# Kernel optimization log

Measured on AMD Instinct MI355X. Metric: run time of the kernel, lower is better.

Reference implementation:

```python
import jax, jax.numpy as jnp
import numpy as np

N_ATOM = 4_000_000
N_FRAG = 200_000
EIG_THRESHOLD = 0.01


def setup_inputs() -> dict:
    key = jax.random.key(0)
    k1, k2, k3, k4, k5 = jax.random.split(key, 5)
    f_atom = jax.random.normal(k1, (N_ATOM, 3), jnp.float32)
    atom_pos = jax.random.normal(k2, (N_ATOM, 3), jnp.float32) * 5.0
    T_frag = jax.random.normal(k3, (N_FRAG, 3), jnp.float32) * 5.0
    frag_id = jax.random.randint(k4, (N_ATOM,), 0, N_FRAG)
    frag_sizes = jax.random.randint(k5, (N_FRAG,), 1, 40)
    return {"f_atom": f_atom, "atom_pos": atom_pos, "T_frag": T_frag,
            "frag_id": frag_id, "frag_sizes": frag_sizes, "n_frag": N_FRAG}


def reference(f_atom, atom_pos, T_frag, frag_id, frag_sizes, n_frag):
    dtype = f_atom.dtype
    # scatter_mean(f_atom, frag_id): segment_sum / counts
    counts = jax.ops.segment_sum(jnp.ones((f_atom.shape[0],), dtype), frag_id,
                                 num_segments=n_frag)
    denom = jnp.maximum(counts, 1.0)[:, None]
    v_frag = jax.ops.segment_sum(f_atom, frag_id, num_segments=n_frag) / denom  # [F,3]

    r_arm = atom_pos - T_frag[frag_id]                                   # [N,3]
    torque = jax.ops.segment_sum(jnp.cross(r_arm, f_atom), frag_id,
                                 num_segments=n_frag)                    # [F,3]

    r2 = jnp.sum(r_arm * r_arm, axis=-1)                                 # [N]
    I_diag = jax.ops.segment_sum(r2, frag_id, num_segments=n_frag)       # [F]
    rr = r_arm[:, :, None] * r_arm[:, None, :]                           # [N,3,3]
    I_off = jax.ops.segment_sum(rr.reshape(-1, 9), frag_id,
                                num_segments=n_frag).reshape(-1, 3, 3)   # [F,3,3]
    I_tensor = I_diag[:, None, None] * jnp.eye(3, dtype=dtype) - I_off   # [F,3,3]

    eigenvalues, eigenvectors = jnp.linalg.eigh(I_tensor)                # [F,3], [F,3,3]
    max_eig = jnp.maximum(jnp.max(eigenvalues, axis=-1, keepdims=True), 1e-8)
    observable = (eigenvalues > EIG_THRESHOLD * max_eig).astype(dtype)   # [F,3]
    observable = jnp.where((frag_sizes <= 1)[:, None],
                           jnp.zeros((), dtype), observable)

    torque_eig = jnp.einsum('nji,nj->ni', eigenvectors, torque)          # V^T torque
    omega_eig = torque_eig / jnp.maximum(eigenvalues, 1e-6) * observable
    omega_frag = jnp.einsum('nij,nj->ni', eigenvectors, omega_eig)
    P_observable = jnp.einsum('nij,nj,nkj->nik', eigenvectors, observable, eigenvectors)
    return v_frag, omega_frag, P_observable
```

## Files before the change

### kernel.cpp

```cpp
#include <hip/hip_runtime.h>
#include <math.h>

__device__ __forceinline__ void frag_epilogue(
    const float* a, int f, int n_frag, const int* __restrict__ frag_sizes,
    float* __restrict__ out)
{
    float cntf  = a[12];
    float denom = fmaxf(cntf, 1.0f);
    float vfx = a[0] / denom, vfy = a[1] / denom, vfz = a[2] / denom;

    double tq0 = (double)a[3], tq1 = (double)a[4], tq2 = (double)a[5];
    double Mxx = (double)a[6], Myy = (double)a[7], Mzz = (double)a[8];
    double Mxy = (double)a[9], Mxz = (double)a[10], Myz = (double)a[11];
    double tr = Mxx + Myy + Mzz;

    double A[3][3] = {
        { tr - Mxx, -Mxy,     -Mxz     },
        { -Mxy,     tr - Myy, -Myz     },
        { -Mxz,     -Myz,     tr - Mzz }
    };
    double V[3][3] = {{1,0,0},{0,1,0},{0,0,1}};

    for (int sweep = 0; sweep < 6; ++sweep) {
        for (int pq = 0; pq < 3; ++pq) {
            int p = (pq == 2) ? 1 : 0;
            int q = (pq == 0) ? 1 : 2;
            double apq = A[p][q];
            if (fabs(apq) <= 1e-14 * (fabs(A[p][p]) + fabs(A[q][q])) ||
                fabs(apq) < 1e-300) continue;
            double theta = (A[q][q] - A[p][p]) / (2.0 * apq);
            double tt;
            if (fabs(theta) > 1e100) tt = 1.0 / (2.0 * theta);
            else tt = copysign(1.0, theta) / (fabs(theta) + sqrt(theta * theta + 1.0));
            double c = 1.0 / sqrt(tt * tt + 1.0);
            double s = tt * c;
            double app = A[p][p], aqq = A[q][q];
            A[p][p] = app - tt * apq;
            A[q][q] = aqq + tt * apq;
            A[p][q] = 0.0; A[q][p] = 0.0;
            int r = 3 - p - q;
            double arp = A[r][p], arq = A[r][q];
            A[r][p] = c * arp - s * arq; A[p][r] = A[r][p];
            A[r][q] = s * arp + c * arq; A[q][r] = A[r][q];
            for (int i2 = 0; i2 < 3; ++i2) {
                double vip = V[i2][p], viq = V[i2][q];
                V[i2][p] = c * vip - s * viq;
                V[i2][q] = s * vip + c * viq;
            }
        }
    }

    double lam0 = A[0][0], lam1 = A[1][1], lam2 = A[2][2];
    double maxeig = fmax(fmax(fmax(lam0, lam1), lam2), 1e-8);
    double thr = 0.01 * maxeig;
    bool small_frag = (frag_sizes[f] <= 1);
    double o0 = (!small_frag && lam0 > thr) ? 1.0 : 0.0;
    double o1 = (!small_frag && lam1 > thr) ? 1.0 : 0.0;
    double o2 = (!small_frag && lam2 > thr) ? 1.0 : 0.0;

    double te0 = V[0][0]*tq0 + V[1][0]*tq1 + V[2][0]*tq2;
    double te1 = V[0][1]*tq0 + V[1][1]*tq1 + V[2][1]*tq2;
    double te2 = V[0][2]*tq0 + V[1][2]*tq1 + V[2][2]*tq2;
    double we0 = te0 / fmax(lam0, 1e-6) * o0;
    double we1 = te1 / fmax(lam1, 1e-6) * o1;
    double we2 = te2 / fmax(lam2, 1e-6) * o2;
    double w0 = V[0][0]*we0 + V[0][1]*we1 + V[0][2]*we2;
    double w1 = V[1][0]*we0 + V[1][1]*we1 + V[1][2]*we2;
    double w2 = V[2][0]*we0 + V[2][1]*we1 + V[2][2]*we2;

    size_t F = (size_t)n_frag;
    out[(size_t)f*3 + 0] = vfx;
    out[(size_t)f*3 + 1] = vfy;
    out[(size_t)f*3 + 2] = vfz;
    out[F*3 + (size_t)f*3 + 0] = (float)w0;
    out[F*3 + (size_t)f*3 + 1] = (float)w1;
    out[F*3 + (size_t)f*3 + 2] = (float)w2;

    float* P = out + F*6 + (size_t)f*9;
    #pragma unroll
    for (int i2 = 0; i2 < 3; ++i2)
        #pragma unroll
        for (int k = 0; k < 3; ++k)
            P[i2*3 + k] = (float)(V[i2][0]*o0*V[k][0] + V[i2][1]*o1*V[k][1]
                                  + V[i2][2]*o2*V[k][2]);
}

#define NBK  512
#define FPB  400
#define CAP2 2048
#define TILE 16
#define APB  (256 * TILE)
#define MAXPT 8
#define NCHUNK 16

__global__ __launch_bounds__(256) void count_atoms(
    const int* __restrict__ frag_id,
    unsigned*  __restrict__ histrows,
    int n_atom)
{
    __shared__ unsigned hist[NBK];
    int t = threadIdx.x;
    for (int b = t; b < NBK; b += 256) hist[b] = 0;
    __syncthreads();
    const int4* fid4 = (const int4*)frag_id;
    int bs4 = blockIdx.x * (APB / 4);
    #pragma unroll
    for (int j = 0; j < TILE / 4; ++j) {
        int i4 = bs4 + j * 256 + t;
        if (4 * i4 < n_atom) {
            int4 v = fid4[i4];
            atomicAdd(&hist[v.x / FPB], 1u);
            atomicAdd(&hist[v.y / FPB], 1u);
            atomicAdd(&hist[v.z / FPB], 1u);
            atomicAdd(&hist[v.w / FPB], 1u);
        }
    }
    __syncthreads();
    unsigned* row = histrows + (size_t)blockIdx.x * NBK;
    for (int b = t; b < NBK; b += 256) row[b] = hist[b];
}

__global__ __launch_bounds__(256) void scan_pass1(
    const unsigned* __restrict__ histrows,
    unsigned* __restrict__ chunksums,
    int nblk, int ch)
{
    int col = blockIdx.x * 256 + threadIdx.x;
    int c   = blockIdx.y;
    int r0 = c * ch, r1 = r0 + ch;
    if (r1 > nblk) r1 = nblk;
    unsigned s = 0;
    for (int r = r0; r < r1; ++r) s += histrows[(size_t)r * NBK + col];
    chunksums[(size_t)c * NBK + col] = s;
}

__global__ __launch_bounds__(256) void scan_pass2(
    unsigned* __restrict__ chunksums,
    unsigned* __restrict__ totals)
{
    int col = blockIdx.x * 256 + threadIdx.x;
    unsigned cum = 0;
    #pragma unroll
    for (int c = 0; c < NCHUNK; ++c) {
        size_t idx = (size_t)c * NBK + col;
        unsigned v = chunksums[idx];
        chunksums[idx] = cum;
        cum += v;
    }
    totals[col] = cum;
}

__global__ __launch_bounds__(256) void scan_pass3(
    unsigned* __restrict__ histrows,
    const unsigned* __restrict__ chunksums,
    int nblk, int ch)
{
    int col = blockIdx.x * 256 + threadIdx.x;
    int c   = blockIdx.y;
    int r0 = c * ch, r1 = r0 + ch;
    if (r1 > nblk) r1 = nblk;
    unsigned cum = chunksums[(size_t)c * NBK + col];
    for (int r = r0; r < r1; ++r) {
        size_t idx = (size_t)r * NBK + col;
        unsigned v = histrows[idx];
        histrows[idx] = cum;
        cum += v;
    }
}

__global__ __launch_bounds__(256) void scan_base(
    const unsigned* __restrict__ totals,
    unsigned* __restrict__ bucket_base)
{
    __shared__ unsigned part[256];
    int t = threadIdx.x;
    unsigned v0 = totals[2*t], v1 = totals[2*t + 1];
    part[t] = v0 + v1;
    __syncthreads();
    for (int st = 1; st < 256; st <<= 1) {
        unsigned v = (t >= st) ? part[t - st] : 0u;
        __syncthreads();
        part[t] += v;
        __syncthreads();
    }
    unsigned base = (t == 0) ? 0u : part[t - 1];
    bucket_base[2*t]     = base;
    bucket_base[2*t + 1] = base + v0;
    if (t == 255) bucket_base[NBK] = part[255];
}

__global__ __launch_bounds__(256) void scatter_atoms(
    const float* __restrict__ f_atom,
    const float* __restrict__ atom_pos,
    const int*   __restrict__ frag_id,
    const unsigned* __restrict__ histrows,
    const unsigned* __restrict__ bucket_base,
    float4*      __restrict__ recs,
    int n_atom)
{
    __shared__ unsigned hist[NBK];
    __shared__ unsigned obase[NBK];
    int t = threadIdx.x;
    for (int b = t; b < NBK; b += 256) hist[b] = 0;
    __syncthreads();

    const int4*   fid4 = (const int4*)frag_id;
    const float4* pos4 = (const float4*)atom_pos;
    const float4* ff4  = (const float4*)f_atom;
    int bs4 = blockIdx.x * (APB / 4);

    int4     fv[TILE / 4];
    unsigned rank[TILE];
    #pragma unroll
    for (int j = 0; j < TILE / 4; ++j) {
        int i4 = bs4 + j * 256 + t;
        if (4 * i4 < n_atom) {
            int4 v = fid4[i4];
            fv[j] = v;
            rank[4*j+0] = atomicAdd(&hist[v.x / FPB], 1u);
            rank[4*j+1] = atomicAdd(&hist[v.y / FPB], 1u);
            rank[4*j+2] = atomicAdd(&hist[v.z / FPB], 1u);
            rank[4*j+3] = atomicAdd(&hist[v.w / FPB], 1u);
        } else {
            fv[j].x = -1;
        }
    }
    const unsigned* row = histrows + (size_t)blockIdx.x * NBK;
    for (int b = t; b < NBK; b += 256) obase[b] = row[b] + bucket_base[b];
    __syncthreads();

    #pragma unroll
    for (int j = 0; j < TILE / 4; ++j) {
        if (fv[j].x < 0) continue;
        size_t i4 = (size_t)(bs4 + j * 256 + t);
        float4 p0 = pos4[3*i4+0], p1 = pos4[3*i4+1], p2 = pos4[3*i4+2];
        float4 g0 = ff4[3*i4+0],  g1 = ff4[3*i4+1],  g2 = ff4[3*i4+2];
        float px[4] = {p0.x, p0.w, p1.z, p2.y};
        float py[4] = {p0.y, p1.x, p1.w, p2.z};
        float pz[4] = {p0.z, p1.y, p2.x, p2.w};
        float gx[4] = {g0.x, g0.w, g1.z, g2.y};
        float gy[4] = {g0.y, g1.x, g1.w, g2.z};
        float gz[4] = {g0.z, g1.y, g2.x, g2.w};
        int fid_[4] = {fv[j].x, fv[j].y, fv[j].z, fv[j].w};
        #pragma unroll
        for (int c = 0; c < 4; ++c) {
            int fid = fid_[c];
            int bk = fid / FPB;
            int lf = fid - bk * FPB;
            unsigned pos = obase[bk] + rank[4*j + c];
            recs[2*(size_t)pos + 0] = make_float4(px[c], py[c], pz[c], __int_as_float(lf));
            recs[2*(size_t)pos + 1] = make_float4(gx[c], gy[c], gz[c], 0.0f);
        }
    }
}

__global__ __launch_bounds__(256) void sort_reduce(
    const float4*   __restrict__ recs,
    const unsigned* __restrict__ bucket_base,
    const float*    __restrict__ T_frag,
    const int*      __restrict__ frag_sizes,
    float*          __restrict__ out,
    int n_frag)
{
    __shared__ float    srt[CAP2 * 7];
    __shared__ unsigned hist[FPB];
    __shared__ unsigned sc[256];
    __shared__ unsigned cbase[FPB];

    int b = blockIdx.x, t = threadIdx.x;
    int frag0 = b * FPB;
    int nf = n_frag - frag0;
    if (nf > FPB) nf = FPB;

    unsigned start = bucket_base[b];
    unsigned end   = bucket_base[b + 1];

    bool v0 = (t < nf);
    bool v1 = (256 + t < nf);
    float T0x=0,T0y=0,T0z=0, T1x=0,T1y=0,T1z=0;
    if (v0) { int f = frag0 + t;       T0x=T_frag[3*f]; T0y=T_frag[3*f+1]; T0z=T_frag[3*f+2]; }
    if (v1) { int f = frag0 + 256 + t; T1x=T_frag[3*f]; T1y=T_frag[3*f+1]; T1z=T_frag[3*f+2]; }

    float s0[12], s1[12];
    #pragma unroll
    for (int k = 0; k < 12; ++k) { s0[k] = 0.0f; s1[k] = 0.0f; }
    unsigned c0n = 0, c1n = 0;

    for (unsigned c0 = start; c0 < end; c0 += CAP2) {
        unsigned m = end - c0;
        if (m > CAP2) m = CAP2;

        for (int k = t; k < FPB; k += 256) hist[k] = 0;
        __syncthreads();

        float4 rv[MAXPT], fvv[MAXPT];
        int rlf[MAXPT];
        unsigned rrk[MAXPT];
        #pragma unroll
        for (int k = 0; k < MAXPT; ++k) {
            unsigned i = (unsigned)t + (unsigned)k * 256u;
            rlf[k] = -1;
            if (i < m) {
                rv[k]  = recs[2 * (size_t)(c0 + i) + 0];
                fvv[k] = recs[2 * (size_t)(c0 + i) + 1];
                int lf = __float_as_int(rv[k].w);
                rlf[k] = lf;
                rrk[k] = atomicAdd(&hist[lf], 1u);
            }
        }
        __syncthreads();

        unsigned p = 0;
        if (2 * t < FPB) p = hist[2*t] + hist[2*t + 1];
        sc[t] = p;
        __syncthreads();
        #pragma unroll
        for (int st = 1; st < 256; st <<= 1) {
            unsigned v = (t >= st) ? sc[t - st] : 0u;
            __syncthreads();
            sc[t] += v;
            __syncthreads();
        }
        if (2 * t < FPB) {
            unsigned excl = sc[t] - p;
            cbase[2*t]     = excl;
            cbase[2*t + 1] = excl + hist[2*t];
        }
        __syncthreads();

        #pragma unroll
        for (int k = 0; k < MAXPT; ++k) {
            if (rlf[k] >= 0) {
                unsigned q = (cbase[rlf[k]] + rrk[k]) * 7u;
                srt[q + 0] = rv[k].x;  srt[q + 1] = rv[k].y;  srt[q + 2] = rv[k].z;
                srt[q + 3] = fvv[k].x; srt[q + 4] = fvv[k].y; srt[q + 5] = fvv[k].z;
            }
        }
        __syncthreads();

        if (v0) {
            unsigned cb = cbase[t], cnt = hist[t];
            c0n += cnt;
            for (unsigned k = 0; k < cnt; ++k) {
                const float* d = &srt[(cb + k) * 7u];
                float rx = d[0] - T0x, ry = d[1] - T0y, rz = d[2] - T0z;
                float Fx = d[3], Fy = d[4], Fz = d[5];
                s0[0] += Fx; s0[1] += Fy; s0[2] += Fz;
                s0[3] += ry*Fz - rz*Fy;
                s0[4] += rz*Fx - rx*Fz;
                s0[5] += rx*Fy - ry*Fx;
                s0[6] += rx*rx; s0[7] += ry*ry; s0[8] += rz*rz;
                s0[9] += rx*ry; s0[10] += rx*rz; s0[11] += ry*rz;
            }
        }
        if (v1) {
            unsigned cb = cbase[256 + t], cnt = hist[256 + t];
            c1n += cnt;
            for (unsigned k = 0; k < cnt; ++k) {
                const float* d = &srt[(cb + k) * 7u];
                float rx = d[0] - T1x, ry = d[1] - T1y, rz = d[2] - T1z;
                float Fx = d[3], Fy = d[4], Fz = d[5];
                s1[0] += Fx; s1[1] += Fy; s1[2] += Fz;
                s1[3] += ry*Fz - rz*Fy;
                s1[4] += rz*Fx - rx*Fz;
                s1[5] += rx*Fy - ry*Fx;
                s1[6] += rx*rx; s1[7] += ry*ry; s1[8] += rz*rz;
                s1[9] += rx*ry; s1[10] += rx*rz; s1[11] += ry*rz;
            }
        }
        __syncthreads();
    }

    if (v0) {
        float a[13];
        #pragma unroll
        for (int k = 0; k < 12; ++k) a[k] = s0[k];
        a[12] = (float)c0n;
        frag_epilogue(a, frag0 + t, n_frag, frag_sizes, out);
    }
    if (v1) {
        float a[13];
        #pragma unroll
        for (int k = 0; k < 12; ++k) a[k] = s1[k];
        a[12] = (float)c1n;
        frag_epilogue(a, frag0 + 256 + t, n_frag, frag_sizes, out);
    }
}

#define NACC 16

__global__ __launch_bounds__(256) void atom_scatter_fb(
    const float* __restrict__ f_atom, const float* __restrict__ atom_pos,
    const float* __restrict__ T_frag, const int* __restrict__ frag_id,
    float* __restrict__ acc, int n_atom)
{
    int i = blockIdx.x * blockDim.x + threadIdx.x;
    if (i >= n_atom) return;
    int fid = frag_id[i];
    float fx = f_atom[3*i+0], fy = f_atom[3*i+1], fz = f_atom[3*i+2];
    float px = atom_pos[3*i+0], py = atom_pos[3*i+1], pz = atom_pos[3*i+2];
    float rx = px - T_frag[3*fid+0], ry = py - T_frag[3*fid+1], rz = pz - T_frag[3*fid+2];
    float cx = ry*fz - rz*fy, cy = rz*fx - rx*fz, cz = rx*fy - ry*fx;
    float* a = acc + (size_t)fid * NACC;
    atomicAdd(a+0, fx);    atomicAdd(a+1, fy);    atomicAdd(a+2, fz);
    atomicAdd(a+3, cx);    atomicAdd(a+4, cy);    atomicAdd(a+5, cz);
    atomicAdd(a+6, rx*rx); atomicAdd(a+7, ry*ry); atomicAdd(a+8, rz*rz);
    atomicAdd(a+9, rx*ry); atomicAdd(a+10, rx*rz); atomicAdd(a+11, ry*rz);
    atomicAdd(a+12, 1.0f);
}

__global__ __launch_bounds__(256) void frag_solve_fb(
    const float* __restrict__ acc, const int* __restrict__ frag_sizes,
    float* __restrict__ out, int n_frag)
{
    int f = blockIdx.x * blockDim.x + threadIdx.x;
    if (f >= n_frag) return;
    float a[13];
    #pragma unroll
    for (int k = 0; k < 13; ++k) a[k] = acc[(size_t)f * NACC + k];
    frag_epilogue(a, f, n_frag, frag_sizes, out);
}

extern "C" void kernel_launch(void* const* d_in, const int* in_sizes, int n_in,
                              void* d_out, int out_size, void* d_ws, size_t ws_size,
                              hipStream_t stream) {
    const float* f_atom     = (const float*)d_in[0];
    const float* atom_pos   = (const float*)d_in[1];
    const float* T_frag     = (const float*)d_in[2];
    const int*   frag_id    = (const int*)d_in[3];
    const int*   frag_sizes = (const int*)d_in[4];
    int n_atom = in_sizes[0] / 3;
    int n_frag = in_sizes[2] / 3;
    float* out = (float*)d_out;

    int nblk = (n_atom + APB - 1) / APB;
    int nbk  = (n_frag + FPB - 1) / FPB;
    int ch   = (nblk + NCHUNK - 1) / NCHUNK;

    size_t hist_bytes = (size_t)nblk * NBK * sizeof(unsigned);
    size_t cs_off     = hist_bytes;
    size_t tot_off    = cs_off + (size_t)NCHUNK * NBK * sizeof(unsigned);
    size_t base_off   = tot_off + NBK * sizeof(unsigned);
    size_t recs_off   = (base_off + (NBK + 1) * sizeof(unsigned) + 255) & ~(size_t)255;
    size_t need       = recs_off + (size_t)n_atom * 2 * sizeof(float4);

    if (ws_size >= need && nbk <= NBK && (n_atom % 4) == 0) {
        unsigned* histrows    = (unsigned*)d_ws;
        unsigned* chunksums   = (unsigned*)((char*)d_ws + cs_off);
        unsigned* totals      = (unsigned*)((char*)d_ws + tot_off);
        unsigned* bucket_base = (unsigned*)((char*)d_ws + base_off);
        float4*   recs        = (float4*)((char*)d_ws + recs_off);

        count_atoms<<<nblk, 256, 0, stream>>>(frag_id, histrows, n_atom);
        dim3 sgrid(NBK / 256, NCHUNK);
        scan_pass1<<<sgrid, 256, 0, stream>>>(histrows, chunksums, nblk, ch);
        scan_pass2<<<NBK / 256, 256, 0, stream>>>(chunksums, totals);
        scan_base<<<1, 256, 0, stream>>>(totals, bucket_base);
        scan_pass3<<<sgrid, 256, 0, stream>>>(histrows, chunksums, nblk, ch);
        scatter_atoms<<<nblk, 256, 0, stream>>>(
            f_atom, atom_pos, frag_id, histrows, bucket_base, recs, n_atom);
        sort_reduce<<<nbk, 256, 0, stream>>>(
            recs, bucket_base, T_frag, frag_sizes, out, n_frag);
    } else {
        float* acc = (float*)d_ws;
        hipMemsetAsync(acc, 0, (size_t)n_frag * NACC * sizeof(float), stream);
        atom_scatter_fb<<<(n_atom + 255) / 256, 256, 0, stream>>>(
            f_atom, atom_pos, T_frag, frag_id, acc, n_atom);
        frag_solve_fb<<<(n_frag + 255) / 256, 256, 0, stream>>>(acc, frag_sizes, out, n_frag);
    }
}
```

Before: 275.2 us.

## Locally sort atom chunks in LDS before scattering records to buckets

The scatter kernel now processes each block's atoms in chunks of 2048. It ranks them per bucket with LDS atomics, prefix-scans the chunk histogram, and stages records in shared memory sorted by bucket. Records are then written out with consecutive threads targeting consecutive addresses within each bucket, so global writes are more contiguous than the previous random per-atom scatter. The cost is extra LDS traffic, a 256-step scan with many barriers per chunk, and higher shared memory use, which may lower occupancy.

```diff
diff --git a/kernel.cpp b/kernel.cpp
--- a/kernel.cpp
+++ b/kernel.cpp
@@ -92,6 +92,8 @@
 #define APB  (256 * TILE)
 #define MAXPT 8
 #define NCHUNK 16
+#define SCHUNK 2048
+#define CPT    8
 
 __global__ __launch_bounds__(256) void count_atoms(
     const int* __restrict__ frag_id,
@@ -198,59 +200,108 @@
     float4*      __restrict__ recs,
     int n_atom)
 {
+    __shared__ float    srt[SCHUNK * 7];
     __shared__ unsigned hist[NBK];
+    __shared__ unsigned cbase[NBK];
     __shared__ unsigned obase[NBK];
+    __shared__ unsigned sc[256];
     int t = threadIdx.x;
-    for (int b = t; b < NBK; b += 256) hist[b] = 0;
-    __syncthreads();
+
+    const unsigned* row = histrows + (size_t)blockIdx.x * NBK;
+    for (int b = t; b < NBK; b += 256) obase[b] = row[b] + bucket_base[b];
 
     const int4*   fid4 = (const int4*)frag_id;
     const float4* pos4 = (const float4*)atom_pos;
     const float4* ff4  = (const float4*)f_atom;
-    int bs4 = blockIdx.x * (APB / 4);
-
-    int4     fv[TILE / 4];
-    unsigned rank[TILE];
-    #pragma unroll
-    for (int j = 0; j < TILE / 4; ++j) {
-        int i4 = bs4 + j * 256 + t;
-        if (4 * i4 < n_atom) {
-            int4 v = fid4[i4];
-            fv[j] = v;
-            rank[4*j+0] = atomicAdd(&hist[v.x / FPB], 1u);
-            rank[4*j+1] = atomicAdd(&hist[v.y / FPB], 1u);
-            rank[4*j+2] = atomicAdd(&hist[v.z / FPB], 1u);
-            rank[4*j+3] = atomicAdd(&hist[v.w / FPB], 1u);
-        } else {
-            fv[j].x = -1;
-        }
-    }
-    const unsigned* row = histrows + (size_t)blockIdx.x * NBK;
-    for (int b = t; b < NBK; b += 256) obase[b] = row[b] + bucket_base[b];
-    __syncthreads();
-
-    #pragma unroll
-    for (int j = 0; j < TILE / 4; ++j) {
-        if (fv[j].x < 0) continue;
-        size_t i4 = (size_t)(bs4 + j * 256 + t);
-        float4 p0 = pos4[3*i4+0], p1 = pos4[3*i4+1], p2 = pos4[3*i4+2];
-        float4 g0 = ff4[3*i4+0],  g1 = ff4[3*i4+1],  g2 = ff4[3*i4+2];
-        float px[4] = {p0.x, p0.w, p1.z, p2.y};
-        float py[4] = {p0.y, p1.x, p1.w, p2.z};
-        float pz[4] = {p0.z, p1.y, p2.x, p2.w};
-        float gx[4] = {g0.x, g0.w, g1.z, g2.y};
-        float gy[4] = {g0.y, g1.x, g1.w, g2.z};
-        float gz[4] = {g0.z, g1.y, g2.x, g2.w};
-        int fid_[4] = {fv[j].x, fv[j].y, fv[j].z, fv[j].w};
-        #pragma unroll
-        for (int c = 0; c < 4; ++c) {
-            int fid = fid_[c];
-            int bk = fid / FPB;
-            int lf = fid - bk * FPB;
-            unsigned pos = obase[bk] + rank[4*j + c];
-            recs[2*(size_t)pos + 0] = make_float4(px[c], py[c], pz[c], __int_as_float(lf));
-            recs[2*(size_t)pos + 1] = make_float4(gx[c], gy[c], gz[c], 0.0f);
-        }
+    int bs = blockIdx.x * APB;
+
+    for (int c = 0; c < APB / SCHUNK; ++c) {
+        int cs = bs + c * SCHUNK;
+        int mchunk = n_atom - cs;
+        if (mchunk > SCHUNK) mchunk = SCHUNK;
+        if (mchunk < 0) mchunk = 0;
+
+        for (int b = t; b < NBK; b += 256) hist[b] = 0;
+        __syncthreads();
+
+        int      bkv[CPT], lfv[CPT];
+        unsigned rk[CPT];
+        float ax[CPT], ay[CPT], az[CPT], gx[CPT], gy[CPT], gz[CPT];
+        #pragma unroll
+        for (int q = 0; q < CPT / 4; ++q) {
+            int i4 = (cs >> 2) + q * 256 + t;
+            if (4 * i4 < n_atom) {
+                int4 v = fid4[i4];
+                float4 p0 = pos4[3*(size_t)i4+0], p1 = pos4[3*(size_t)i4+1], p2 = pos4[3*(size_t)i4+2];
+                float4 g0 = ff4[3*(size_t)i4+0],  g1 = ff4[3*(size_t)i4+1],  g2 = ff4[3*(size_t)i4+2];
+                int   fid_[4] = {v.x, v.y, v.z, v.w};
+                float px_[4] = {p0.x, p0.w, p1.z, p2.y};
+                float py_[4] = {p0.y, p1.x, p1.w, p2.z};
+                float pz_[4] = {p0.z, p1.y, p2.x, p2.w};
+                float gx_[4] = {g0.x, g0.w, g1.z, g2.y};
+                float gy_[4] = {g0.y, g1.x, g1.w, g2.z};
+                float gz_[4] = {g0.z, g1.y, g2.x, g2.w};
+                #pragma unroll
+                for (int cc = 0; cc < 4; ++cc) {
+                    int k = q * 4 + cc;
+                    int fid = fid_[cc];
+                    int bk = fid / FPB;
+                    bkv[k] = bk;
+                    lfv[k] = fid - bk * FPB;
+                    rk[k]  = atomicAdd(&hist[bk], 1u);
+                    ax[k] = px_[cc]; ay[k] = py_[cc]; az[k] = pz_[cc];
+                    gx[k] = gx_[cc]; gy[k] = gy_[cc]; gz[k] = gz_[cc];
+                }
+            } else {
+                #pragma unroll
+                for (int cc = 0; cc < 4; ++cc) bkv[q * 4 + cc] = -1;
+            }
+        }
+        __syncthreads();
+
+        unsigned pv = hist[2*t] + hist[2*t + 1];
+        sc[t] = pv;
+        __syncthreads();
+        #pragma unroll
+        for (int st = 1; st < 256; st <<= 1) {
+            unsigned v = (t >= st) ? sc[t - st] : 0u;
+            __syncthreads();
+            sc[t] += v;
+            __syncthreads();
+        }
+        unsigned excl = sc[t] - pv;
+        cbase[2*t]     = excl;
+        cbase[2*t + 1] = excl + hist[2*t];
+        __syncthreads();
+
+        #pragma unroll
+        for (int k = 0; k < CPT; ++k) {
+            if (bkv[k] >= 0) {
+                unsigned p = (cbase[bkv[k]] + rk[k]) * 7u;
+                srt[p+0] = ax[k]; srt[p+1] = ay[k]; srt[p+2] = az[k];
+                srt[p+3] = gx[k]; srt[p+4] = gy[k]; srt[p+5] = gz[k];
+                srt[p+6] = __int_as_float(lfv[k] | (bkv[k] << 16));
+            }
+        }
+        __syncthreads();
+
+        #pragma unroll
+        for (int k = 0; k < CPT; ++k) {
+            int j = t + k * 256;
+            if (j < mchunk) {
+                const float* d = &srt[(unsigned)j * 7u];
+                int pk = __float_as_int(d[6]);
+                int lf = pk & 0xFFFF;
+                int bk = pk >> 16;
+                unsigned addr = obase[bk] + (unsigned)j - cbase[bk];
+                recs[2*(size_t)addr + 0] = make_float4(d[0], d[1], d[2], __int_as_float(lf));
+                recs[2*(size_t)addr + 1] = make_float4(d[3], d[4], d[5], 0.0f);
+            }
+        }
+        __syncthreads();
+
+        for (int b = t; b < NBK; b += 256) obase[b] += hist[b];
+        __syncthreads();
     }
 }
 
```

Result: faster. 254.9 us (-7.4%).
